# Performance work log

Hardware: AMD Instinct MI355X
Metric: run time of the kernel (lower is better)

The kernel has to match this reference:

```python
import jax, jax.numpy as jnp
import numpy as np

B, S, E = 8, 2048, 1024


def setup_inputs() -> dict:
    key = jax.random.key(0)
    ks = jax.random.split(key, 8)
    scale = 1.0 / np.sqrt(E)
    x = jax.random.normal(ks[0], (B, S, E), dtype=jnp.float32)
    Wq = jax.random.uniform(ks[1], (E, E), jnp.float32, -scale, scale)
    bq = jax.random.uniform(ks[2], (E,), jnp.float32, -scale, scale)
    Wk = jax.random.uniform(ks[3], (E, E), jnp.float32, -scale, scale)
    bk = jax.random.uniform(ks[4], (E,), jnp.float32, -scale, scale)
    Wv = jax.random.uniform(ks[5], (E, E), jnp.float32, -scale, scale)
    bv = jax.random.uniform(ks[6], (E,), jnp.float32, -scale, scale)
    # key-padding mask: True = fill position (broadcasts over query dim)
    mask = jax.random.randint(ks[7], (B, 1, S), 0, 2) > 0
    return {"x": x, "Wq": Wq, "bq": bq, "Wk": Wk, "bk": bk, "Wv": Wv, "bv": bv, "mask": mask}


def reference(x, Wq, bq, Wk, bk, Wv, bv, mask):
    # torch Linear: y = x @ W.T + b
    q = jnp.einsum('bse,fe->bsf', x, Wq) + bq
    k = jnp.einsum('bse,fe->bsf', x, Wk) + bk
    v = jnp.einsum('bse,fe->bsf', x, Wv) + bv
    inv_sqrt_d = 1.0 / jnp.sqrt(jnp.asarray(E, x.dtype))
    A = jnp.einsum('bqe,bke->bqk', q, k) * inv_sqrt_d  # (B, S, S)
    # non-standard masked_fill: fills with 1e-9 (NOT -inf), pre-softmax
    A = jnp.where(mask, jnp.asarray(1e-9, A.dtype), A)
    A = jax.nn.softmax(A, axis=-1)
    out = jnp.einsum('bqk,bke->bqe', A, v)
    # dropout is identity at inference
    return out
```

## Files before the change

kernel.cpp:

```cpp
#include <hip/hip_runtime.h>
#include <hip/hip_bf16.h>

#define B_ 8
#define S_ 2048
#define E_ 1024

using f32x4 = __attribute__((ext_vector_type(4))) float;
using s16x8 = __attribute__((ext_vector_type(8))) short;
using u16x8 = __attribute__((ext_vector_type(8))) unsigned short;

typedef __attribute__((address_space(1))) unsigned int glb_u32;
typedef __attribute__((address_space(3))) unsigned int lds_u32;

#define FENCE() __builtin_amdgcn_sched_barrier(0)

static __device__ __forceinline__ unsigned short f2bf(float f) {
    union { float f; unsigned int u; } v; v.f = f;
    unsigned int u = v.u;
    u += 0x7FFFu + ((u >> 16) & 1u);
    return (unsigned short)(u >> 16);
}
static __device__ __forceinline__ float bf2f(unsigned short h) {
    union { unsigned int u; float f; } v; v.u = ((unsigned int)h) << 16;
    return v.f;
}

__global__ __launch_bounds__(256) void mask_canon_kernel(
    const unsigned char* __restrict__ src, unsigned char* __restrict__ dst, int n)
{
    __shared__ int flags;
    if (threadIdx.x == 0) flags = 0;
    __syncthreads();
    int f = 0;
    for (int j = threadIdx.x; j < n; j += 256) {
        unsigned char b = src[j];
        if (b) {
            int p = j & 3;
            if (p == 1) f |= 1;
            if (p >= 2) f |= 2;
        }
    }
    if (f) atomicOr(&flags, f);
    __syncthreads();
    const int fl = flags;
    for (int i = threadIdx.x; i < n; i += 256) {
        unsigned char v;
        if (fl & 1)      v = (unsigned char)(src[i] != 0);
        else if (fl & 2) v = (unsigned char)(((const float*)(const void*)src)[i] != 0.0f);
        else             v = (unsigned char)(((const int*)(const void*)src)[i] != 0);
        dst[i] = v;
    }
}

__global__ __launch_bounds__(256) void cvt_all_kernel(
    const float* __restrict__ x,  unsigned short* __restrict__ xb,
    const float* __restrict__ w0, unsigned short* __restrict__ d0,
    const float* __restrict__ w1, unsigned short* __restrict__ d1,
    const float* __restrict__ w2, unsigned short* __restrict__ d2,
    int nx8, int nw8)
{
    const int total = nx8 + 3 * nw8;
    const int stride = gridDim.x * 256;
    for (int i = blockIdx.x * 256 + threadIdx.x; i < total; i += stride) {
        const float* s; unsigned short* d; int k;
        if (i < nx8)                { s = x;  d = xb; k = i; }
        else if (i < nx8 + nw8)     { s = w0; d = d0; k = i - nx8; }
        else if (i < nx8 + 2 * nw8) { s = w1; d = d1; k = i - nx8 - nw8; }
        else                        { s = w2; d = d2; k = i - nx8 - 2 * nw8; }
        float4 a = *(const float4*)(s + (size_t)k * 8);
        float4 b = *(const float4*)(s + (size_t)k * 8 + 4);
        u16x8 o;
        o[0]=f2bf(a.x); o[1]=f2bf(a.y); o[2]=f2bf(a.z); o[3]=f2bf(a.w);
        o[4]=f2bf(b.x); o[5]=f2bf(b.y); o[6]=f2bf(b.z); o[7]=f2bf(b.w);
        *(u16x8*)(d + (size_t)k * 8) = o;
    }
}

template<int EPI>
__global__ __launch_bounds__(512, 2) void gemm256(
    const unsigned short* __restrict__ A, const unsigned short* __restrict__ B,
    void* __restrict__ Cout,
    long long sAz, long long sBz, long long sCz,
    int lda, int ldb, int ldc, int K,
    const unsigned char* __restrict__ mask, int maskStride, float scale,
    const float* __restrict__ bias,
    const unsigned short* __restrict__ B2, const float* __restrict__ bias2,
    void* __restrict__ Cout2, float* __restrict__ aux)
{
    __shared__ unsigned short lds[65536];
    const int tid = threadIdx.x;
    const int lane = tid & 63, w = tid >> 6;
    const int wr = w >> 2, wc = w & 3;
    const int fr = lane & 15, ch = lane >> 4;

    const int gx = gridDim.x, gy = gridDim.y;
    const int nwg = gx * gy * gridDim.z;
    int bid = blockIdx.x + gx * (blockIdx.y + gy * blockIdx.z);
    bid = (bid & 7) * (nwg >> 3) + (bid >> 3);
    const int bx = bid % gx; int tmp = bid / gx;
    const int by = tmp % gy; const int bz = tmp / gy;

    const unsigned short* Ab = A + (size_t)bz * sAz;
    const unsigned short* Bb = B + (size_t)bz * sBz;
    const float* biasv = bias;
    void* Coutv = Cout;
    const int m0 = by * 256;
    int n0 = bx * 256;
    if constexpr (EPI == 4) {
        if (n0 >= 1024) { Bb = B2; biasv = bias2; Coutv = Cout2; n0 -= 1024; }
    }

    const int rdlane = fr * 32 + ((ch * 8) ^ ((fr & 8) ? 16 : 0));
    const int local = (lane * 16) ^ (lane & 32);
    const int rloc = local >> 6;
    const int cloc = (local >> 4) & 3;

    f32x4 acc[8][4] = {};
    const int NT = K >> 6;

    auto STAGE = [&](const unsigned short* __restrict__ src, int ld, int base,
                     int ts, int half, int matoff, unsigned bo) {
        const int k0 = ts * 64;
        const int rowb = half * 128 + w * 16;
        #pragma unroll
        for (int kk = 0; kk < 2; ++kk) {
            const unsigned short* g = src + (size_t)(base + rowb + rloc) * ld
                                          + (k0 + kk * 32 + cloc * 8);
            __builtin_amdgcn_global_load_lds((const glb_u32*)g,
                (lds_u32*)&lds[bo + matoff + kk * 8192 + rowb * 32], 16, 0, 0);
        }
    };

    STAGE(Ab, lda, m0, 0, 0, 0, 0);      STAGE(Ab, lda, m0, 0, 1, 0, 0);
    STAGE(Bb, ldb, n0, 0, 0, 16384, 0);  STAGE(Bb, ldb, n0, 0, 1, 16384, 0);
    STAGE(Ab, lda, m0, 1, 0, 0, 32768);  STAGE(Ab, lda, m0, 1, 1, 0, 32768);
    STAGE(Bb, ldb, n0, 1, 0, 16384, 32768);
    asm volatile("s_waitcnt vmcnt(6)" ::: "memory");
    __builtin_amdgcn_s_barrier();

    for (int t = 0; t < NT; ++t) {
        const unsigned bo = (unsigned)(t & 1) * 32768u;
        const unsigned nbo = bo ^ 32768u;
        const int tp1 = (t + 1 < NT) ? t + 1 : NT - 1;
        const int tp2 = (t + 2 < NT) ? t + 2 : NT - 1;

        s16x8 af[8][2], bfv[4][2];
        #pragma unroll
        for (int i = 0; i < 4; ++i)
            #pragma unroll
            for (int kk = 0; kk < 2; ++kk)
                af[i][kk] = *(const s16x8*)&lds[bo + kk * 8192 + (wr * 128 + i * 16) * 32 + rdlane];
        #pragma unroll
        for (int j = 0; j < 2; ++j)
            #pragma unroll
            for (int kk = 0; kk < 2; ++kk)
                bfv[j][kk] = *(const s16x8*)&lds[bo + 16384 + kk * 8192 + (wc * 64 + j * 16) * 32 + rdlane];
        FENCE();
        #pragma unroll
        for (int i = 4; i < 8; ++i)
            #pragma unroll
            for (int kk = 0; kk < 2; ++kk)
                af[i][kk] = *(const s16x8*)&lds[bo + kk * 8192 + (wr * 128 + i * 16) * 32 + rdlane];
        #pragma unroll
        for (int j = 2; j < 4; ++j)
            #pragma unroll
            for (int kk = 0; kk < 2; ++kk)
                bfv[j][kk] = *(const s16x8*)&lds[bo + 16384 + kk * 8192 + (wc * 64 + j * 16) * 32 + rdlane];
        STAGE(Bb, ldb, n0, tp1, 1, 16384, nbo);
        FENCE();
        asm volatile("s_waitcnt lgkmcnt(12)" ::: "memory");
        FENCE();
        __builtin_amdgcn_s_setprio(1);
        #pragma unroll
        for (int kk = 0; kk < 2; ++kk)
            #pragma unroll
            for (int i = 0; i < 4; ++i)
                #pragma unroll
                for (int j = 0; j < 2; ++j)
                    acc[i][j] = __builtin_amdgcn_mfma_f32_16x16x32_bf16(af[i][kk], bfv[j][kk], acc[i][j], 0, 0, 0);
        __builtin_amdgcn_s_setprio(0);
        FENCE();
        asm volatile("s_waitcnt lgkmcnt(0)" ::: "memory");
        FENCE();
        __builtin_amdgcn_s_setprio(1);
        #pragma unroll
        for (int kk = 0; kk < 2; ++kk)
            #pragma unroll
            for (int i = 0; i < 4; ++i)
                #pragma unroll
                for (int j = 0; j < 2; ++j)
                    acc[i][2 + j] = __builtin_amdgcn_mfma_f32_16x16x32_bf16(af[i][kk], bfv[2 + j][kk], acc[i][2 + j], 0, 0, 0);
        __builtin_amdgcn_s_setprio(0);
        FENCE();
        __builtin_amdgcn_s_barrier();
        FENCE();
        STAGE(Bb, ldb, n0, tp2, 0, 16384, bo);
        STAGE(Ab, lda, m0, tp2, 0, 0, bo);
        STAGE(Ab, lda, m0, tp2, 1, 0, bo);
        FENCE();
        __builtin_amdgcn_s_setprio(1);
        #pragma unroll
        for (int kk = 0; kk < 2; ++kk)
            #pragma unroll
            for (int i = 0; i < 4; ++i)
                #pragma unroll
                for (int j = 0; j < 2; ++j)
                    acc[4 + i][j] = __builtin_amdgcn_mfma_f32_16x16x32_bf16(af[4 + i][kk], bfv[j][kk], acc[4 + i][j], 0, 0, 0);
        #pragma unroll
        for (int kk = 0; kk < 2; ++kk)
            #pragma unroll
            for (int i = 0; i < 4; ++i)
                #pragma unroll
                for (int j = 0; j < 2; ++j)
                    acc[4 + i][2 + j] = __builtin_amdgcn_mfma_f32_16x16x32_bf16(af[4 + i][kk], bfv[2 + j][kk], acc[4 + i][2 + j], 0, 0, 0);
        __builtin_amdgcn_s_setprio(0);
        FENCE();
        asm volatile("s_waitcnt vmcnt(6)" ::: "memory");
        FENCE();
        __builtin_amdgcn_s_barrier();
    }

    asm volatile("s_waitcnt vmcnt(0) lgkmcnt(0)" ::: "memory");
    __builtin_amdgcn_s_barrier();

    if constexpr (EPI == 1) {
        float* Cb = (float*)Coutv + (size_t)bz * sCz;
        float* lf = (float*)lds;
        #pragma unroll
        for (int p = 0; p < 2; ++p) {
            if (p == 1) __syncthreads();
            #pragma unroll
            for (int j = 0; j < 4; ++j) {
                const int lcol = wc * 64 + j * 16 + fr;
                #pragma unroll
                for (int i = 0; i < 4; ++i)
                    #pragma unroll
                    for (int r = 0; r < 4; ++r) {
                        const int lrow = wr * 64 + i * 16 + ch * 4 + r;
                        lf[lrow * 256 + lcol] = acc[4 * p + i][j][r];
                    }
            }
            __syncthreads();
            #pragma unroll
            for (int s = 0; s < 16; ++s) {
                const int lrow = s * 8 + (tid >> 6);
                const int colf = (tid & 63) * 4;
                float4 v = *(const float4*)&lf[lrow * 256 + colf];
                const int mrow = m0 + ((lrow >= 64) ? 128 : 0) + p * 64 + (lrow & 63);
                const float* pp = aux + ((size_t)bz * S_ + mrow) * 8;
                const float ssum = ((pp[0] + pp[1]) + (pp[2] + pp[3]))
                                 + ((pp[4] + pp[5]) + (pp[6] + pp[7]));
                const float irs = 1.0f / ssum;
                v.x *= irs; v.y *= irs; v.z *= irs; v.w *= irs;
                *(float4*)&Cb[(size_t)mrow * ldc + n0 + colf] = v;
            }
        }
    } else {
        unsigned short* Cb = (unsigned short*)Coutv + (size_t)bz * sCz;
        const unsigned char* mb = (EPI == 0) ? mask + (size_t)bz * maskStride : nullptr;
        #pragma unroll
        for (int j = 0; j < 4; ++j) {
            const int lcol = wc * 64 + j * 16 + fr;
            bool msk = false; float bn = 0.f;
            if constexpr (EPI == 0) msk = mb[n0 + lcol] != 0;
            if constexpr (EPI == 2 || EPI == 4) bn = biasv[n0 + lcol];
            #pragma unroll
            for (int i = 0; i < 8; ++i) {
                #pragma unroll
                for (int r = 0; r < 4; ++r) {
                    const int lrow = wr * 128 + i * 16 + ch * 4 + r;
                    float val;
                    if constexpr (EPI == 0)      val = msk ? 1.0f : __expf(acc[i][j][r] * scale);
                    else if constexpr (EPI == 2 || EPI == 4) val = acc[i][j][r] + bn;
                    else                         val = acc[i][j][r] + biasv[m0 + lrow];
                    lds[lrow * 256 + lcol] = f2bf(val);
                }
            }
        }
        __syncthreads();
        if constexpr (EPI == 0) {
            const int row = tid >> 1, half = tid & 1;
            float s = 0.f;
            #pragma unroll
            for (int c = 0; c < 16; ++c) {
                const int cc = (c + row) & 15;
                u16x8 v8 = *(const u16x8*)&lds[row * 256 + half * 128 + cc * 8];
                #pragma unroll
                for (int e = 0; e < 8; ++e) s += bf2f(v8[e]);
            }
            s += __shfl_xor(s, 1, 64);
            if (half == 0)
                aux[((size_t)bz * S_ + m0 + row) * 8 + bx] = s;
        }
        #pragma unroll
        for (int s = 0; s < 16; ++s) {
            const int lrow = s * 16 + (tid >> 5);
            const int colu = (tid & 31) * 8;
            u16x8 v = *(const u16x8*)&lds[lrow * 256 + colu];
            *(u16x8*)&Cb[(size_t)(m0 + lrow) * ldc + n0 + colu] = v;
        }
    }
}

extern "C" void kernel_launch(void* const* d_in, const int* in_sizes, int n_in,
                              void* d_out, int out_size, void* d_ws, size_t ws_size,
                              hipStream_t stream)
{
    const float* x  = (const float*)d_in[0];
    const float* Wq = (const float*)d_in[1];
    const float* bq = (const float*)d_in[2];
    const float* Wk = (const float*)d_in[3];
    const float* bk = (const float*)d_in[4];
    const float* Wv = (const float*)d_in[5];
    const float* bv = (const float*)d_in[6];
    const unsigned char* mraw = (const unsigned char*)d_in[7];

    const int BS = B_ * S_;
    unsigned short* Qb = (unsigned short*)d_ws;
    unsigned short* Kb = Qb + (size_t)BS * E_;
    unsigned short* VT = Kb + (size_t)BS * E_;
    unsigned short* Sc = VT + (size_t)BS * E_;
    unsigned short* xb = Sc;
    unsigned short* Wqb = Sc + (size_t)BS * E_;
    unsigned short* Wkb = Wqb + (size_t)E_ * E_;
    unsigned short* Wvb = Wkb + (size_t)E_ * E_;
    unsigned char* mcanon = (unsigned char*)(Sc + (size_t)B_ * S_ * S_);
    float* psum = (float*)(mcanon + 65536);

    mask_canon_kernel<<<1, 256, 0, stream>>>(mraw, mcanon, BS);

    cvt_all_kernel<<<2048, 256, 0, stream>>>(
        x, xb, Wq, Wqb, Wk, Wkb, Wv, Wvb, BS * E_ / 8, E_ * E_ / 8);

    gemm256<4><<<dim3(2048 / 256, BS / 256), 512, 0, stream>>>(
        xb, Wqb, (void*)Qb, 0, 0, 0, E_, E_, E_, E_, nullptr, 0, 1.0f, bq,
        Wkb, bk, (void*)Kb, nullptr);
    gemm256<3><<<dim3(BS / 256, E_ / 256), 512, 0, stream>>>(
        Wvb, xb, (void*)VT, 0, 0, 0, E_, E_, BS, E_, nullptr, 0, 1.0f, bv,
        nullptr, nullptr, nullptr, nullptr);

    gemm256<0><<<dim3(S_ / 256, S_ / 256, B_), 512, 0, stream>>>(
        Qb, Kb, (void*)Sc,
        (long long)S_ * E_, (long long)S_ * E_, (long long)S_ * S_,
        E_, E_, S_, E_, mcanon, S_, 0.03125f, nullptr,
        nullptr, nullptr, nullptr, psum);

    gemm256<1><<<dim3(E_ / 256, S_ / 256, B_), 512, 0, stream>>>(
        Sc, VT, d_out,
        (long long)S_ * S_, (long long)S_, (long long)S_ * E_,
        S_, BS, E_, S_, nullptr, 0, 1.0f, nullptr,
        nullptr, nullptr, nullptr, psum);
}
```

Baseline: 307.2 us.

## Split attention GEMMs into 1024-thread kernel with triple-buffered BK=32 pipeline

The two batched attention GEMMs (QK^T with exp/mask epilogue and PV with normalization) move to a new kernel using 16 waves per 256x256 tile. Each wave owns a 64x64 sub-tile, the K-step drops to 32, and staging uses three rotating LDS buffers with global_load_lds. This spreads the tile across more waves and reduces per-wave accumulator registers to hide latency better. The epilogues are adapted to the new wave layout, and the projection GEMMs keep the old kernel under a new name. In exchange, each wave does less MFMA work per LDS read, and there are more barriers per K iteration.

```diff
diff --git a/kernel.cpp b/kernel.cpp
--- a/kernel.cpp
+++ b/kernel.cpp
@@ -77,15 +77,13 @@
 }
 
 template<int EPI>
-__global__ __launch_bounds__(512, 2) void gemm256(
+__global__ __launch_bounds__(512, 2) void gemm_proj(
     const unsigned short* __restrict__ A, const unsigned short* __restrict__ B,
     void* __restrict__ Cout,
-    long long sAz, long long sBz, long long sCz,
     int lda, int ldb, int ldc, int K,
-    const unsigned char* __restrict__ mask, int maskStride, float scale,
     const float* __restrict__ bias,
     const unsigned short* __restrict__ B2, const float* __restrict__ bias2,
-    void* __restrict__ Cout2, float* __restrict__ aux)
+    void* __restrict__ Cout2)
 {
     __shared__ unsigned short lds[65536];
     const int tid = threadIdx.x;
@@ -94,14 +92,13 @@
     const int fr = lane & 15, ch = lane >> 4;
 
     const int gx = gridDim.x, gy = gridDim.y;
-    const int nwg = gx * gy * gridDim.z;
-    int bid = blockIdx.x + gx * (blockIdx.y + gy * blockIdx.z);
+    const int nwg = gx * gy;
+    int bid = blockIdx.x + gx * blockIdx.y;
     bid = (bid & 7) * (nwg >> 3) + (bid >> 3);
-    const int bx = bid % gx; int tmp = bid / gx;
-    const int by = tmp % gy; const int bz = tmp / gy;
-
-    const unsigned short* Ab = A + (size_t)bz * sAz;
-    const unsigned short* Bb = B + (size_t)bz * sBz;
+    const int bx = bid % gx; const int by = bid / gx;
+
+    const unsigned short* Ab = A;
+    const unsigned short* Bb = B;
     const float* biasv = bias;
     void* Coutv = Cout;
     const int m0 = by * 256;
@@ -223,30 +220,170 @@
     asm volatile("s_waitcnt vmcnt(0) lgkmcnt(0)" ::: "memory");
     __builtin_amdgcn_s_barrier();
 
+    unsigned short* Cb = (unsigned short*)Coutv;
+    #pragma unroll
+    for (int j = 0; j < 4; ++j) {
+        const int lcol = wc * 64 + j * 16 + fr;
+        float bn = 0.f;
+        if constexpr (EPI == 4) bn = biasv[n0 + lcol];
+        #pragma unroll
+        for (int i = 0; i < 8; ++i) {
+            #pragma unroll
+            for (int r = 0; r < 4; ++r) {
+                const int lrow = wr * 128 + i * 16 + ch * 4 + r;
+                float val;
+                if constexpr (EPI == 4) val = acc[i][j][r] + bn;
+                else                    val = acc[i][j][r] + biasv[m0 + lrow];
+                lds[lrow * 256 + lcol] = f2bf(val);
+            }
+        }
+    }
+    __syncthreads();
+    #pragma unroll
+    for (int s = 0; s < 16; ++s) {
+        const int lrow = s * 16 + (tid >> 5);
+        const int colu = (tid & 31) * 8;
+        u16x8 v = *(const u16x8*)&lds[lrow * 256 + colu];
+        *(u16x8*)&Cb[(size_t)(m0 + lrow) * ldc + n0 + colu] = v;
+    }
+}
+
+template<int EPI>
+__global__ __launch_bounds__(1024, 4) void gemm_attn(
+    const unsigned short* __restrict__ A, const unsigned short* __restrict__ B,
+    void* __restrict__ Cout,
+    long long sAz, long long sBz, long long sCz,
+    int lda, int ldb, int ldc, int K,
+    const unsigned char* __restrict__ mask, float scale,
+    float* __restrict__ aux)
+{
+    __shared__ unsigned short lds[65536];
+    const int tid = threadIdx.x;
+    const int lane = tid & 63, w = tid >> 6;
+    const int wr = w >> 2, wc = w & 3;
+    const int fr = lane & 15, ch = lane >> 4;
+
+    const int gx = gridDim.x, gy = gridDim.y;
+    const int nwg = gx * gy * gridDim.z;
+    int bid = blockIdx.x + gx * (blockIdx.y + gy * blockIdx.z);
+    bid = (bid & 7) * (nwg >> 3) + (bid >> 3);
+    const int bx = bid % gx; int tmp = bid / gx;
+    const int by = tmp % gy; const int bz = tmp / gy;
+
+    const unsigned short* Ab = A + (size_t)bz * sAz;
+    const unsigned short* Bb = B + (size_t)bz * sBz;
+    const int m0 = by * 256, n0 = bx * 256;
+
+    const int rdlane = fr * 32 + ((ch * 8) ^ ((fr & 8) ? 16 : 0));
+    const int local = (lane * 16) ^ (lane & 32);
+    const int rloc = local >> 6;
+    const int cloc = (local >> 4) & 3;
+
+    f32x4 acc[4][4] = {};
+    const int NT = K >> 5;
+
+    const unsigned short* ssrc = (w < 8) ? Ab : Bb;
+    const int sld   = (w < 8) ? lda : ldb;
+    const int sbase = (w < 8) ? m0 : n0;
+    const int smat  = (w < 8) ? 0 : 8192;
+    const int srow0 = (w & 7) * 32;
+
+    auto STAGE_TILE = [&](int ts, unsigned bufo) {
+        #pragma unroll
+        for (int half = 0; half < 2; ++half) {
+            const int rowb = srow0 + half * 16;
+            const unsigned short* g = ssrc + (size_t)(sbase + rowb + rloc) * sld
+                                          + (ts * 32 + cloc * 8);
+            __builtin_amdgcn_global_load_lds((const glb_u32*)g,
+                (lds_u32*)&lds[bufo + smat + rowb * 32], 16, 0, 0);
+        }
+    };
+
+    STAGE_TILE(0, 0);
+    STAGE_TILE((1 < NT) ? 1 : 0, 16384);
+    asm volatile("s_waitcnt vmcnt(2)" ::: "memory");
+    __builtin_amdgcn_s_barrier();
+
+    unsigned cur = 0, nxt = 16384, stg = 32768;
+    for (int t = 0; t < NT; ++t) {
+        const int tp2 = (t + 2 < NT) ? t + 2 : NT - 1;
+
+        s16x8 af[4], bfv[4];
+        #pragma unroll
+        for (int i = 0; i < 2; ++i)
+            af[i] = *(const s16x8*)&lds[cur + (wr * 64 + i * 16) * 32 + rdlane];
+        #pragma unroll
+        for (int j = 0; j < 2; ++j)
+            bfv[j] = *(const s16x8*)&lds[cur + 8192 + (wc * 64 + j * 16) * 32 + rdlane];
+        FENCE();
+        #pragma unroll
+        for (int i = 2; i < 4; ++i)
+            af[i] = *(const s16x8*)&lds[cur + (wr * 64 + i * 16) * 32 + rdlane];
+        #pragma unroll
+        for (int j = 2; j < 4; ++j)
+            bfv[j] = *(const s16x8*)&lds[cur + 8192 + (wc * 64 + j * 16) * 32 + rdlane];
+        STAGE_TILE(tp2, stg);
+        FENCE();
+        asm volatile("s_waitcnt lgkmcnt(4)" ::: "memory");
+        FENCE();
+        __builtin_amdgcn_s_setprio(1);
+        #pragma unroll
+        for (int i = 0; i < 2; ++i)
+            #pragma unroll
+            for (int j = 0; j < 2; ++j)
+                acc[i][j] = __builtin_amdgcn_mfma_f32_16x16x32_bf16(af[i], bfv[j], acc[i][j], 0, 0, 0);
+        __builtin_amdgcn_s_setprio(0);
+        FENCE();
+        asm volatile("s_waitcnt lgkmcnt(0)" ::: "memory");
+        FENCE();
+        __builtin_amdgcn_s_setprio(1);
+        #pragma unroll
+        for (int i = 0; i < 2; ++i)
+            #pragma unroll
+            for (int j = 2; j < 4; ++j)
+                acc[i][j] = __builtin_amdgcn_mfma_f32_16x16x32_bf16(af[i], bfv[j], acc[i][j], 0, 0, 0);
+        #pragma unroll
+        for (int i = 2; i < 4; ++i)
+            #pragma unroll
+            for (int j = 0; j < 4; ++j)
+                acc[i][j] = __builtin_amdgcn_mfma_f32_16x16x32_bf16(af[i], bfv[j], acc[i][j], 0, 0, 0);
+        __builtin_amdgcn_s_setprio(0);
+        FENCE();
+        asm volatile("s_waitcnt vmcnt(2)" ::: "memory");
+        FENCE();
+        __builtin_amdgcn_s_barrier();
+        const unsigned tmpb = cur; cur = nxt; nxt = stg; stg = tmpb;
+    }
+
+    asm volatile("s_waitcnt vmcnt(0) lgkmcnt(0)" ::: "memory");
+    __builtin_amdgcn_s_barrier();
+
     if constexpr (EPI == 1) {
-        float* Cb = (float*)Coutv + (size_t)bz * sCz;
+        float* Cb = (float*)Cout + (size_t)bz * sCz;
         float* lf = (float*)lds;
         #pragma unroll
         for (int p = 0; p < 2; ++p) {
             if (p == 1) __syncthreads();
-            #pragma unroll
-            for (int j = 0; j < 4; ++j) {
-                const int lcol = wc * 64 + j * 16 + fr;
-                #pragma unroll
-                for (int i = 0; i < 4; ++i)
+            if ((wr >> 1) == p) {
+                #pragma unroll
+                for (int j = 0; j < 4; ++j) {
+                    const int lcol = wc * 64 + j * 16 + fr;
                     #pragma unroll
-                    for (int r = 0; r < 4; ++r) {
-                        const int lrow = wr * 64 + i * 16 + ch * 4 + r;
-                        lf[lrow * 256 + lcol] = acc[4 * p + i][j][r];
-                    }
+                    for (int i = 0; i < 4; ++i)
+                        #pragma unroll
+                        for (int r = 0; r < 4; ++r) {
+                            const int lrow = (wr & 1) * 64 + i * 16 + ch * 4 + r;
+                            lf[lrow * 256 + lcol] = acc[i][j][r];
+                        }
+                }
             }
             __syncthreads();
             #pragma unroll
-            for (int s = 0; s < 16; ++s) {
-                const int lrow = s * 8 + (tid >> 6);
+            for (int s = 0; s < 8; ++s) {
+                const int lrow = s * 16 + (tid >> 6);
                 const int colf = (tid & 63) * 4;
                 float4 v = *(const float4*)&lf[lrow * 256 + colf];
-                const int mrow = m0 + ((lrow >= 64) ? 128 : 0) + p * 64 + (lrow & 63);
+                const int mrow = m0 + p * 128 + lrow;
                 const float* pp = aux + ((size_t)bz * S_ + mrow) * 8;
                 const float ssum = ((pp[0] + pp[1]) + (pp[2] + pp[3]))
                                  + ((pp[4] + pp[5]) + (pp[6] + pp[7]));
@@ -256,45 +393,41 @@
             }
         }
     } else {
-        unsigned short* Cb = (unsigned short*)Coutv + (size_t)bz * sCz;
-        const unsigned char* mb = (EPI == 0) ? mask + (size_t)bz * maskStride : nullptr;
+        unsigned short* Cb = (unsigned short*)Cout + (size_t)bz * sCz;
+        const unsigned char* mb = mask + (size_t)bz * S_;
         #pragma unroll
         for (int j = 0; j < 4; ++j) {
             const int lcol = wc * 64 + j * 16 + fr;
-            bool msk = false; float bn = 0.f;
-            if constexpr (EPI == 0) msk = mb[n0 + lcol] != 0;
-            if constexpr (EPI == 2 || EPI == 4) bn = biasv[n0 + lcol];
-            #pragma unroll
-            for (int i = 0; i < 8; ++i) {
+            const bool msk = mb[n0 + lcol] != 0;
+            #pragma unroll
+            for (int i = 0; i < 4; ++i) {
                 #pragma unroll
                 for (int r = 0; r < 4; ++r) {
-                    const int lrow = wr * 128 + i * 16 + ch * 4 + r;
-                    float val;
-                    if constexpr (EPI == 0)      val = msk ? 1.0f : __expf(acc[i][j][r] * scale);
-                    else if constexpr (EPI == 2 || EPI == 4) val = acc[i][j][r] + bn;
-                    else                         val = acc[i][j][r] + biasv[m0 + lrow];
+                    const int lrow = wr * 64 + i * 16 + ch * 4 + r;
+                    const float val = msk ? 1.0f : __expf(acc[i][j][r] * scale);
                     lds[lrow * 256 + lcol] = f2bf(val);
                 }
             }
         }
         __syncthreads();
-        if constexpr (EPI == 0) {
-            const int row = tid >> 1, half = tid & 1;
+        {
+            const int row = tid >> 2, q = tid & 3;
             float s = 0.f;
             #pragma unroll
-            for (int c = 0; c < 16; ++c) {
-                const int cc = (c + row) & 15;
-                u16x8 v8 = *(const u16x8*)&lds[row * 256 + half * 128 + cc * 8];
+            for (int c = 0; c < 8; ++c) {
+                const int cc = (c + row) & 7;
+                u16x8 v8 = *(const u16x8*)&lds[row * 256 + q * 64 + cc * 8];
                 #pragma unroll
                 for (int e = 0; e < 8; ++e) s += bf2f(v8[e]);
             }
             s += __shfl_xor(s, 1, 64);
-            if (half == 0)
+            s += __shfl_xor(s, 2, 64);
+            if (q == 0)
                 aux[((size_t)bz * S_ + m0 + row) * 8 + bx] = s;
         }
         #pragma unroll
-        for (int s = 0; s < 16; ++s) {
-            const int lrow = s * 16 + (tid >> 5);
+        for (int s = 0; s < 8; ++s) {
+            const int lrow = s * 32 + (tid >> 5);
             const int colu = (tid & 31) * 8;
             u16x8 v = *(const u16x8*)&lds[lrow * 256 + colu];
             *(u16x8*)&Cb[(size_t)(m0 + lrow) * ldc + n0 + colu] = v;
@@ -332,22 +465,18 @@
     cvt_all_kernel<<<2048, 256, 0, stream>>>(
         x, xb, Wq, Wqb, Wk, Wkb, Wv, Wvb, BS * E_ / 8, E_ * E_ / 8);
 
-    gemm256<4><<<dim3(2048 / 256, BS / 256), 512, 0, stream>>>(
-        xb, Wqb, (void*)Qb, 0, 0, 0, E_, E_, E_, E_, nullptr, 0, 1.0f, bq,
-        Wkb, bk, (void*)Kb, nullptr);
-    gemm256<3><<<dim3(BS / 256, E_ / 256), 512, 0, stream>>>(
-        Wvb, xb, (void*)VT, 0, 0, 0, E_, E_, BS, E_, nullptr, 0, 1.0f, bv,
-        nullptr, nullptr, nullptr, nullptr);
-
-    gemm256<0><<<dim3(S_ / 256, S_ / 256, B_), 512, 0, stream>>>(
+    gemm_proj<4><<<dim3(2048 / 256, BS / 256), 512, 0, stream>>>(
+        xb, Wqb, (void*)Qb, E_, E_, E_, E_, bq, Wkb, bk, (void*)Kb);
+    gemm_proj<3><<<dim3(BS / 256, E_ / 256), 512, 0, stream>>>(
+        Wvb, xb, (void*)VT, E_, E_, BS, E_, bv, nullptr, nullptr, nullptr);
+
+    gemm_attn<0><<<dim3(S_ / 256, S_ / 256, B_), 1024, 0, stream>>>(
         Qb, Kb, (void*)Sc,
         (long long)S_ * E_, (long long)S_ * E_, (long long)S_ * S_,
-        E_, E_, S_, E_, mcanon, S_, 0.03125f, nullptr,
-        nullptr, nullptr, nullptr, psum);
-
-    gemm256<1><<<dim3(E_ / 256, S_ / 256, B_), 512, 0, stream>>>(
+        E_, E_, S_, E_, mcanon, 0.03125f, psum);
+
+    gemm_attn<1><<<dim3(E_ / 256, S_ / 256, B_), 1024, 0, stream>>>(
         Sc, VT, d_out,
         (long long)S_ * S_, (long long)S_, (long long)S_ * E_,
-        S_, BS, E_, S_, nullptr, 0, 1.0f, nullptr,
-        nullptr, nullptr, nullptr, psum);
-}
+        S_, BS, E_, S_, nullptr, 1.0f, psum);
+}
```

Measured after the change: 316.3 us. 1.03x slower.
